# Optimization experiments

Hardware: AMD Instinct MI355X
Metric: run time of the kernel (lower is better)

The kernel has to match this reference:

```python
import jax, jax.numpy as jnp
import numpy as np

B, L, H, D = 1024, 32, 64, 2  # batch, lattice size, hiddenSize, inputDim (depth=1)
LOGP_FACTOR = 0.5


def setup_inputs() -> dict:
    key = jax.random.key(0)
    k0, k1, k2, k3 = jax.random.split(key, 4)
    x = jax.random.randint(k0, (B, L, L), 0, D, dtype=jnp.int32)
    # variance_scaling(fan_avg, uniform): limit = sqrt(3*scale / fan_avg)
    lim_in = float(np.sqrt(6.0 / (D + H)))
    lim_c = float(np.sqrt(3.0 / H))
    lim_out = float(np.sqrt(6.0 / (H + D)))
    Win = jax.random.uniform(k1, (D, H), jnp.float32, -lim_in, lim_in)
    Wc = jax.random.uniform(k2, (H, H), jnp.float32, -lim_c, lim_c)
    bc = jnp.zeros((H,), jnp.float32)
    Wout = jax.random.uniform(k3, (H, D), jnp.float32, -lim_out, lim_out)
    bout = jnp.zeros((D,), jnp.float32)
    return {"x": x, "Win": Win, "Wc": Wc, "bc": bc, "Wout": Wout, "bout": bout}


def reference(x, Win, Wc, bc, Wout, bout):
    Ldim = x.shape[-1]
    Hs = Wc.shape[0]
    Dd = Win.shape[0]
    # boustrophedon direction: +1 on even rows, -1 on odd rows
    dnp = np.ones(Ldim, dtype=np.int32)
    dnp[1::2] = -1
    direction = jnp.asarray(dnp)

    def flip_if(a, d):  # reverse_line: identity if d==1 else flip along axis 0
        return jnp.where(d == 1, a, jnp.flip(a, 0))

    def single(xs):  # xs: (L, L) int
        oh = jax.nn.one_hot(xs, Dd, dtype=Win.dtype)  # (L, L, D)

        def col_step(h, cin):
            cV, sH, sV = cin  # (H,), (D,), (D,)
            newR = sH + sV
            newH = jax.nn.elu((h + cV) @ Wc + bc + newR @ Win)  # RNNCell2D
            logits = jax.nn.log_softmax(newH @ Wout + bout)
            return newH, (newH, logits)

        def row_step(carry, row_in):
            prevH, prevOH = carry  # (L, H), (L, D)
            oh_row, d = row_in
            carryV = flip_if(prevH, d)
            stateV = flip_if(prevOH, d)
            stateH = jnp.concatenate(
                [jnp.zeros((1, Dd), oh.dtype), flip_if(oh_row, d)], axis=0)[:-1]
            _, (hs, logps) = jax.lax.scan(
                col_step, jnp.zeros((Hs,), Win.dtype), (carryV, stateH, stateV))
            logp_row = jnp.nan_to_num(
                jnp.sum(flip_if(logps, d) * oh_row, axis=-1), nan=-35.0)
            return (flip_if(hs, d), oh_row), logp_row

        init = (jnp.zeros((Ldim, Hs), Win.dtype), jnp.zeros((Ldim, Dd), Win.dtype))
        _, probs = jax.lax.scan(row_step, init, (oh, direction))
        return LOGP_FACTOR * jnp.sum(probs)

    return jax.vmap(single)(x)  # (B,) log-amplitudes
```

## Files before the change

kernel.cpp:

```cpp
#include <hip/hip_runtime.h>

#define LL 32
#define HH 64

typedef __attribute__((ext_vector_type(4))) float f32x4;

template <int CTRL>
__device__ __forceinline__ float dpp_add_step(float x) {
  int y = __builtin_amdgcn_update_dpp(0, __builtin_bit_cast(int, x), CTRL, 0xf, 0xf, true);
  return x + __builtin_bit_cast(float, y);
}

__device__ __forceinline__ float wave_sum64(float x) {
  x = dpp_add_step<0x111>(x);
  x = dpp_add_step<0x112>(x);
  x = dpp_add_step<0x114>(x);
  x = dpp_add_step<0x118>(x);
  x = dpp_add_step<0x142>(x);
  x = dpp_add_step<0x143>(x);
  return __builtin_bit_cast(float, __builtin_amdgcn_readlane(__builtin_bit_cast(int, x), 63));
}

#define DECL_W(n) float w_##n = Wc[n * HH + lane];
#define LOADG(n) f32x4 g##n = hv4[n];

#define PIN_G4_USE(a, b, c, d) \
  asm volatile("" ::"v"(g##a), "v"(g##b), "v"(g##c), "v"(g##d));

#define MV4(n, i0, i1, i2, i3)        \
  a0 = fmaf(g##n[0], w_##i0, a0);     \
  a1 = fmaf(g##n[1], w_##i1, a1);     \
  a2 = fmaf(g##n[2], w_##i2, a2);     \
  a3 = fmaf(g##n[3], w_##i3, a3);

#define W_OPS_RW                                                               \
  "+v"(w_0), "+v"(w_1), "+v"(w_2), "+v"(w_3), "+v"(w_4), "+v"(w_5),           \
      "+v"(w_6), "+v"(w_7), "+v"(w_8), "+v"(w_9), "+v"(w_10), "+v"(w_11),     \
      "+v"(w_12), "+v"(w_13), "+v"(w_14), "+v"(w_15), "+v"(w_16),             \
      "+v"(w_17), "+v"(w_18), "+v"(w_19), "+v"(w_20), "+v"(w_21),             \
      "+v"(w_22), "+v"(w_23), "+v"(w_24), "+v"(w_25), "+v"(w_26),             \
      "+v"(w_27), "+v"(w_28), "+v"(w_29), "+v"(w_30), "+v"(w_31),             \
      "+v"(w_32), "+v"(w_33), "+v"(w_34), "+v"(w_35), "+v"(w_36),             \
      "+v"(w_37), "+v"(w_38), "+v"(w_39), "+v"(w_40), "+v"(w_41),             \
      "+v"(w_42), "+v"(w_43), "+v"(w_44), "+v"(w_45), "+v"(w_46),             \
      "+v"(w_47), "+v"(w_48), "+v"(w_49), "+v"(w_50), "+v"(w_51),             \
      "+v"(w_52), "+v"(w_53), "+v"(w_54), "+v"(w_55), "+v"(w_56),             \
      "+v"(w_57), "+v"(w_58), "+v"(w_59), "+v"(w_60), "+v"(w_61),             \
      "+v"(w_62), "+v"(w_63), "+v"(win0), "+v"(win1), "+v"(bcj), "+v"(dwout)

#define W_OPS_USE                                                              \
  "v"(w_0), "v"(w_1), "v"(w_2), "v"(w_3), "v"(w_4), "v"(w_5), "v"(w_6),       \
      "v"(w_7), "v"(w_8), "v"(w_9), "v"(w_10), "v"(w_11), "v"(w_12),          \
      "v"(w_13), "v"(w_14), "v"(w_15), "v"(w_16), "v"(w_17), "v"(w_18),       \
      "v"(w_19), "v"(w_20), "v"(w_21), "v"(w_22), "v"(w_23), "v"(w_24),       \
      "v"(w_25), "v"(w_26), "v"(w_27), "v"(w_28), "v"(w_29), "v"(w_30),       \
      "v"(w_31), "v"(w_32), "v"(w_33), "v"(w_34), "v"(w_35), "v"(w_36),       \
      "v"(w_37), "v"(w_38), "v"(w_39), "v"(w_40), "v"(w_41), "v"(w_42),       \
      "v"(w_43), "v"(w_44), "v"(w_45), "v"(w_46), "v"(w_47), "v"(w_48),       \
      "v"(w_49), "v"(w_50), "v"(w_51), "v"(w_52), "v"(w_53), "v"(w_54),       \
      "v"(w_55), "v"(w_56), "v"(w_57), "v"(w_58), "v"(w_59), "v"(w_60),       \
      "v"(w_61), "v"(w_62), "v"(w_63), "v"(win0), "v"(win1), "v"(bcj),        \
      "v"(dwout)

#define PIN_ALL_W_DEF asm volatile("" : W_OPS_RW);
#define PIN_ALL_W_USE asm volatile("" ::W_OPS_USE);

__global__ __launch_bounds__(64, 1) void rnn2d_kernel(
    const int* __restrict__ x, const float* __restrict__ Win,
    const float* __restrict__ Wc, const float* __restrict__ bc,
    const float* __restrict__ Wout, const float* __restrict__ bout,
    float* __restrict__ out) {
  const int lane = threadIdx.x;
  const int b = blockIdx.x;
  __shared__ float vrow[LL * HH];
  __shared__ float hvbuf[2 * HH];

  DECL_W(0)  DECL_W(1)  DECL_W(2)  DECL_W(3)  DECL_W(4)  DECL_W(5)  DECL_W(6)  DECL_W(7)
  DECL_W(8)  DECL_W(9)  DECL_W(10) DECL_W(11) DECL_W(12) DECL_W(13) DECL_W(14) DECL_W(15)
  DECL_W(16) DECL_W(17) DECL_W(18) DECL_W(19) DECL_W(20) DECL_W(21) DECL_W(22) DECL_W(23)
  DECL_W(24) DECL_W(25) DECL_W(26) DECL_W(27) DECL_W(28) DECL_W(29) DECL_W(30) DECL_W(31)
  DECL_W(32) DECL_W(33) DECL_W(34) DECL_W(35) DECL_W(36) DECL_W(37) DECL_W(38) DECL_W(39)
  DECL_W(40) DECL_W(41) DECL_W(42) DECL_W(43) DECL_W(44) DECL_W(45) DECL_W(46) DECL_W(47)
  DECL_W(48) DECL_W(49) DECL_W(50) DECL_W(51) DECL_W(52) DECL_W(53) DECL_W(54) DECL_W(55)
  DECL_W(56) DECL_W(57) DECL_W(58) DECL_W(59) DECL_W(60) DECL_W(61) DECL_W(62) DECL_W(63)

  float win0 = Win[lane];
  float win1 = Win[HH + lane];
  float bcj = bc[lane];
  float dwout = Wout[lane * 2 + 1] - Wout[lane * 2 + 0];
  const float dbout = bout[1] - bout[0];
  PIN_ALL_W_DEF

#pragma unroll
  for (int c0 = 0; c0 < LL; ++c0) vrow[c0 * HH + lane] = 0.f;
  hvbuf[lane] = 0.f;

  const int* xb = x + b * (LL * LL);
  unsigned prevmask = 0u;
  int spv = (lane < LL) ? xb[lane] : 0;
  float total_vec = 0.f;
  float dzbuf = 0.f;

#pragma unroll 1
  for (int r = 0; r < LL; ++r) {
    const unsigned curmask =
        (unsigned)(__ballot(lane < LL && spv) & 0xffffffffull);
    if (r < LL - 1) spv = (lane < LL) ? xb[(r + 1) * LL + lane] : 0;

    PIN_ALL_W_DEF

    const int odd = r & 1;
    const int d = odd ? -1 : 1;
    int c = odd ? (LL - 1) : 0;

#pragma unroll 2
    for (int k = 0; k < LL; ++k) {
      PIN_ALL_W_USE

      const f32x4* hv4 = (const f32x4*)(hvbuf + ((k & 1) ? HH : 0));

      const int cn = (c + d) & (LL - 1);
      const float vjn = vrow[cn * HH + lane];

      LOADG(0)  LOADG(1)  LOADG(2)  LOADG(3)  LOADG(4)  LOADG(5)  LOADG(6)  LOADG(7)
      LOADG(8)  LOADG(9)  LOADG(10) LOADG(11) LOADG(12) LOADG(13) LOADG(14) LOADG(15)

      float a0 = 0.f, a1 = 0.f, a2 = 0.f, a3 = 0.f;
      PIN_G4_USE(0, 1, 2, 3)
      MV4(0, 0, 1, 2, 3)      MV4(1, 4, 5, 6, 7)      MV4(2, 8, 9, 10, 11)
      MV4(3, 12, 13, 14, 15)
      PIN_G4_USE(4, 5, 6, 7)
      MV4(4, 16, 17, 18, 19)  MV4(5, 20, 21, 22, 23)  MV4(6, 24, 25, 26, 27)
      MV4(7, 28, 29, 30, 31)
      PIN_G4_USE(8, 9, 10, 11)
      MV4(8, 32, 33, 34, 35)  MV4(9, 36, 37, 38, 39)  MV4(10, 40, 41, 42, 43)
      MV4(11, 44, 45, 46, 47)
      PIN_G4_USE(12, 13, 14, 15)
      MV4(12, 48, 49, 50, 51) MV4(13, 52, 53, 54, 55) MV4(14, 56, 57, 58, 59)
      MV4(15, 60, 61, 62, 63)

      float winc = 0.f;
      if (k > 0) {
        const unsigned sh = (curmask >> ((c - d) & 31)) & 1u;
        winc += sh ? win1 : win0;
      }
      if (r > 0) {
        const unsigned sv = (prevmask >> c) & 1u;
        winc += sv ? win1 : win0;
      }

      const float pre = ((a0 + a1) + (a2 + a3)) + bcj + winc;
      const float hnew = pre > 0.f ? pre : (__expf(pre) - 1.f);

      vrow[c * HH + lane] = hnew;

      const float hvn = hnew + ((k < LL - 1) ? vjn : 0.f);
      hvbuf[((k & 1) ? 0 : HH) + lane] = hvn;

      const float dzv = wave_sum64(hnew * dwout) + dbout;
      const unsigned spin = (curmask >> c) & 1u;
      const float tv = __builtin_bit_cast(
          float, __builtin_bit_cast(unsigned, dzv) ^ (spin << 31));
      dzbuf = (lane == k) ? tv : dzbuf;

      c = cn;
    }
    prevmask = curmask;

    const float tt = dzbuf;
    float lpv = -(fmaxf(tt, 0.f) + __logf(1.f + __expf(-fabsf(tt))));
    lpv = (lpv == lpv) ? lpv : -35.0f;
    total_vec += (lane < LL) ? lpv : 0.f;
  }

  const float grand = wave_sum64(total_vec);
  if (lane == 0) out[b] = 0.5f * grand;
}

extern "C" void kernel_launch(void* const* d_in, const int* in_sizes, int n_in,
                              void* d_out, int out_size, void* d_ws, size_t ws_size,
                              hipStream_t stream) {
  const int* x = (const int*)d_in[0];
  const float* Win = (const float*)d_in[1];
  const float* Wc = (const float*)d_in[2];
  const float* bc = (const float*)d_in[3];
  const float* Wout = (const float*)d_in[4];
  const float* bout = (const float*)d_in[5];
  float* out = (float*)d_out;
  rnn2d_kernel<<<dim3(out_size), dim3(64), 0, stream>>>(x, Win, Wc, bc, Wout, bout, out);
}
```

Baseline: 407.9 us.

## Replace LDS hidden-state broadcast with DPP wave rotation in matvec

The hidden-state vector stays in a register, one element per lane. Each lane no longer reads all 64 elements back from shared memory. Instead the vector is rotated across the wave one lane at a time with DPP wave_ror, and each lane accumulates against a weight column pre-permuted at load time. This removes the LDS store/load round trip and barrier-free broadcast reads from the serial recurrence. The cost is a 64-step dependent chain of cross-lane moves, which may have its own latency with only one wave per CU.

```diff
diff --git a/kernel.cpp b/kernel.cpp
--- a/kernel.cpp
+++ b/kernel.cpp
@@ -2,14 +2,19 @@
 
 #define LL 32
 #define HH 64
-
-typedef __attribute__((ext_vector_type(4))) float f32x4;
 
 template <int CTRL>
 __device__ __forceinline__ float dpp_add_step(float x) {
   int y = __builtin_amdgcn_update_dpp(0, __builtin_bit_cast(int, x), CTRL, 0xf, 0xf, true);
   return x + __builtin_bit_cast(float, y);
 }
+
+template <int CTRL>
+__device__ __forceinline__ float dpp_mov(float x) {
+  int y = __builtin_amdgcn_update_dpp(0, __builtin_bit_cast(int, x), CTRL, 0xf, 0xf, true);
+  return __builtin_bit_cast(float, y);
+}
+#define WAVE_ROR1(v) dpp_mov<0x13C>(v)
 
 __device__ __forceinline__ float wave_sum64(float x) {
   x = dpp_add_step<0x111>(x);
@@ -21,17 +26,13 @@
   return __builtin_bit_cast(float, __builtin_amdgcn_readlane(__builtin_bit_cast(int, x), 63));
 }
 
-#define DECL_W(n) float w_##n = Wc[n * HH + lane];
-#define LOADG(n) f32x4 g##n = hv4[n];
+#define DECL_W(n) float w_##n = Wc[((lane - n) & 63) * HH + lane];
 
-#define PIN_G4_USE(a, b, c, d) \
-  asm volatile("" ::"v"(g##a), "v"(g##b), "v"(g##c), "v"(g##d));
-
-#define MV4(n, i0, i1, i2, i3)        \
-  a0 = fmaf(g##n[0], w_##i0, a0);     \
-  a1 = fmaf(g##n[1], w_##i1, a1);     \
-  a2 = fmaf(g##n[2], w_##i2, a2);     \
-  a3 = fmaf(g##n[3], w_##i3, a3);
+#define ROT4(t0, t1, t2, t3)                        \
+  a0 = fmaf(v, w_##t0, a0); v = WAVE_ROR1(v);       \
+  a1 = fmaf(v, w_##t1, a1); v = WAVE_ROR1(v);       \
+  a2 = fmaf(v, w_##t2, a2); v = WAVE_ROR1(v);       \
+  a3 = fmaf(v, w_##t3, a3); v = WAVE_ROR1(v);
 
 #define W_OPS_RW                                                               \
   "+v"(w_0), "+v"(w_1), "+v"(w_2), "+v"(w_3), "+v"(w_4), "+v"(w_5),           \
@@ -73,7 +74,6 @@
   const int lane = threadIdx.x;
   const int b = blockIdx.x;
   __shared__ float vrow[LL * HH];
-  __shared__ float hvbuf[2 * HH];
 
   DECL_W(0)  DECL_W(1)  DECL_W(2)  DECL_W(3)  DECL_W(4)  DECL_W(5)  DECL_W(6)  DECL_W(7)
   DECL_W(8)  DECL_W(9)  DECL_W(10) DECL_W(11) DECL_W(12) DECL_W(13) DECL_W(14) DECL_W(15)
@@ -93,13 +93,13 @@
 
 #pragma unroll
   for (int c0 = 0; c0 < LL; ++c0) vrow[c0 * HH + lane] = 0.f;
-  hvbuf[lane] = 0.f;
 
   const int* xb = x + b * (LL * LL);
   unsigned prevmask = 0u;
   int spv = (lane < LL) ? xb[lane] : 0;
   float total_vec = 0.f;
   float dzbuf = 0.f;
+  float hv = 0.f;
 
 #pragma unroll 1
   for (int r = 0; r < LL; ++r) {
@@ -117,27 +117,17 @@
     for (int k = 0; k < LL; ++k) {
       PIN_ALL_W_USE
 
-      const f32x4* hv4 = (const f32x4*)(hvbuf + ((k & 1) ? HH : 0));
+      const int cn = (c + d) & (LL - 1);
+      const float vjn_raw = vrow[cn * HH + lane];
 
-      const int cn = (c + d) & (LL - 1);
-      const float vjn = vrow[cn * HH + lane];
-
-      LOADG(0)  LOADG(1)  LOADG(2)  LOADG(3)  LOADG(4)  LOADG(5)  LOADG(6)  LOADG(7)
-      LOADG(8)  LOADG(9)  LOADG(10) LOADG(11) LOADG(12) LOADG(13) LOADG(14) LOADG(15)
-
+      float v = hv;
       float a0 = 0.f, a1 = 0.f, a2 = 0.f, a3 = 0.f;
-      PIN_G4_USE(0, 1, 2, 3)
-      MV4(0, 0, 1, 2, 3)      MV4(1, 4, 5, 6, 7)      MV4(2, 8, 9, 10, 11)
-      MV4(3, 12, 13, 14, 15)
-      PIN_G4_USE(4, 5, 6, 7)
-      MV4(4, 16, 17, 18, 19)  MV4(5, 20, 21, 22, 23)  MV4(6, 24, 25, 26, 27)
-      MV4(7, 28, 29, 30, 31)
-      PIN_G4_USE(8, 9, 10, 11)
-      MV4(8, 32, 33, 34, 35)  MV4(9, 36, 37, 38, 39)  MV4(10, 40, 41, 42, 43)
-      MV4(11, 44, 45, 46, 47)
-      PIN_G4_USE(12, 13, 14, 15)
-      MV4(12, 48, 49, 50, 51) MV4(13, 52, 53, 54, 55) MV4(14, 56, 57, 58, 59)
-      MV4(15, 60, 61, 62, 63)
+      ROT4(0, 1, 2, 3)      ROT4(4, 5, 6, 7)      ROT4(8, 9, 10, 11)
+      ROT4(12, 13, 14, 15)  ROT4(16, 17, 18, 19)  ROT4(20, 21, 22, 23)
+      ROT4(24, 25, 26, 27)  ROT4(28, 29, 30, 31)  ROT4(32, 33, 34, 35)
+      ROT4(36, 37, 38, 39)  ROT4(40, 41, 42, 43)  ROT4(44, 45, 46, 47)
+      ROT4(48, 49, 50, 51)  ROT4(52, 53, 54, 55)  ROT4(56, 57, 58, 59)
+      ROT4(60, 61, 62, 63)
 
       float winc = 0.f;
       if (k > 0) {
@@ -154,8 +144,8 @@
 
       vrow[c * HH + lane] = hnew;
 
-      const float hvn = hnew + ((k < LL - 1) ? vjn : 0.f);
-      hvbuf[((k & 1) ? 0 : HH) + lane] = hvn;
+      const float vjn = (k < LL - 1) ? vjn_raw : 0.f;
+      hv = hnew + vjn;
 
       const float dzv = wave_sum64(hnew * dwout) + dbout;
       const unsigned spin = (curmask >> c) & 1u;
```

After: 484.7 us. 18.8% more time.
